# Kernel optimization log

Hardware: AMD Instinct MI355X
Metric: run time of the kernel (lower is better)

Reference implementation:

```python
import jax, jax.numpy as jnp
import numpy as np

EPS = 1e-12


def pairwise_sqdist(x, y):
    # x: (B, N, 3), y: (B, M, 3) -> (B, N, M) squared euclidean distances
    xx = jnp.sum(x * x, axis=-1)              # (B, N)
    yy = jnp.sum(y * y, axis=-1)              # (B, M)
    xy = jnp.einsum('bnd,bmd->bnm', x, y)     # (B, N, M)
    d = xx[:, :, None] + yy[None_ if False else yy[:, None, :].shape and 0 or ...] if False else xx[:, :, None] + yy[:, None, :] - 2.0 * xy
    return jnp.maximum(d, 0.0)


def chamfer_l1(x, y):
    # pytorch3d/PoinTr-style ChamferDistanceL1:
    # mean over points of sqrt(min squared dist), averaged over both directions
    d = pairwise_sqdist(x, y)                 # (B, N, M)
    d1 = jnp.min(d, axis=2)                   # (B, N) x -> nearest y
    d2 = jnp.min(d, axis=1)                   # (B, M) y -> nearest x
    d1 = jnp.sqrt(jnp.maximum(d1, EPS))
    d2 = jnp.sqrt(jnp.maximum(d2, EPS))
    return 0.5 * (jnp.mean(d1) + jnp.mean(d2))


def knn1_gather(x, y):
    # For each point in x (B,N,3), find nearest neighbor in y (B,M,3) (K=1)
    # and gather it -> (B, N, 3). Matches knn_points + knn_gather + squeeze.
    d = pairwise_sqdist(x, y)                 # (B, N, M)
    idx = jnp.argmin(d, axis=2)               # (B, N) int
    return jnp.take_along_axis(y, idx[:, :, None], axis=1)  # (B, N, 3)


def volume_with_wedge(p):
    # wedge-product volume over consecutive point triples:
    # V = sum_i (p_i x p_{i+1}) . p_{i+2} / 6  -> (B,)
    c = jnp.cross(p[:, :-2, :], p[:, 1:-1, :])  # (B, N-2, 3)
    return jnp.sum(jnp.einsum('bnd,bnd->bn', c, p[:, 2:, :]), axis=-1) / 6.0


def setup_inputs() -> dict:
    key = jax.random.key(0)
    k1, k2, k3 = jax.random.split(key, 3)
    B, Nc, Nf, M = 2, 512, 8192, 8192
    return {
        'source_coarse': jax.random.normal(k1, (B, Nc, 3), dtype=jnp.float32),
        'source_fine': jax.random.normal(k2, (B, Nf, 3), dtype=jnp.float32),
        'target_points': jax.random.normal(k3, (B, M, 3), dtype=jnp.float32),
    }


def reference(source_coarse, source_fine, target_points):
    lambda_rot = lambda_ref = lambda_align = lambda_geo = 1.0
    B = source_fine.shape[0]
    axis = jnp.broadcast_to(jnp.array([0.0, 0.0, 1.0], dtype=source_fine.dtype), (B, 3))
    plane_normal = jnp.broadcast_to(jnp.array([0.0, 1.0, 0.0], dtype=source_fine.dtype), (B, 3))

    # KNN (K=1) gather of nearest target point for each fine source point
    new_target = knn1_gather(source_fine, target_points)  # (B, Nf, 3)

    # alignment (Chamfer L1) losses
    loss_align_coarse = chamfer_l1(source_coarse, target_points)
    loss_align_fine = chamfer_l1(source_fine, target_points)

    # rotational symmetry loss
    in_proj = jnp.einsum('bij,bj->bi', source_fine, axis)      # (B, Nf)
    re_proj = jnp.einsum('bij,bj->bi', new_target, axis)
    loss_rot = jnp.mean((jnp.linalg.norm(in_proj, axis=-1) - jnp.linalg.norm(re_proj, axis=-1)) ** 2)

    # reflectional symmetry loss
    pn = plane_normal / jnp.linalg.norm(plane_normal, axis=-1, keepdims=True)
    in_dist = jnp.einsum('bij,bj->bi', source_fine, pn)
    re_dist = jnp.einsum('bij,bj->bi', new_target, pn)
    loss_ref = jnp.mean((in_dist - re_dist) ** 2)

    # geometric consistency (wedge-product volume) loss
    loss_geo = jnp.mean((volume_with_wedge(source_fine) - volume_with_wedge(new_target)) ** 2)

    total = (lambda_rot * loss_rot + lambda_ref * loss_ref
             + lambda_align * loss_align_coarse + lambda_align * loss_align_fine
             + lambda_geo * loss_geo)
    return total
```

## Files before the change

### kernel.cpp

```cpp
#include <hip/hip_runtime.h>
#include <stdint.h>

using u64 = unsigned long long;

constexpr int B_ = 2;
constexpr int NC = 512;
constexpr int NF = 8192;
constexpr int MT = 8192;

constexpr int TPB  = 256;
constexpr int RPT  = 2;
constexpr int RPB  = TPB * RPT;
constexpr int TILE = 256;

#define DEVINL __device__ __forceinline__

DEVINL float fmulrn(float a, float b){ return __fmul_rn(a,b); }
DEVINL float faddrn(float a, float b){ return __fadd_rn(a,b); }
DEVINL float fsubrn(float a, float b){ return __fsub_rn(a,b); }

template<bool ARGMIN>
DEVINL void pairmin_body(const float* __restrict__ P, const float* __restrict__ Q,
                         int nP, int nQ, int b, int row_base, int j0,
                         u64* __restrict__ outPack, unsigned* __restrict__ outVal,
                         float4* tile)
{
    const int tid = threadIdx.x;
    float x0[RPT], x1[RPT], x2[RPT], xx[RPT], dbest[RPT];
    int jbest[RPT];
    #pragma unroll
    for (int r = 0; r < RPT; ++r) {
        int row = row_base + tid + r * TPB;
        const float* p = P + ((size_t)b * nP + row) * 3;
        x0[r] = p[0]; x1[r] = p[1]; x2[r] = p[2];
        xx[r] = faddrn(faddrn(fmulrn(x0[r],x0[r]), fmulrn(x1[r],x1[r])),
                       fmulrn(x2[r],x2[r]));
        dbest[r] = __int_as_float(0x7f7fffff);
        jbest[r] = 0;
    }
    {
        const float* q = Q + ((size_t)b * nQ + j0 + tid) * 3;
        float q0 = q[0], q1 = q[1], q2 = q[2];
        float qq = faddrn(faddrn(fmulrn(q0,q0), fmulrn(q1,q1)), fmulrn(q2,q2));
        tile[tid] = make_float4(q0, q1, q2, qq);
    }
    __syncthreads();

    for (int jj = 0; jj < TILE; jj += 4) {
        float4 qv[4];
        #pragma unroll
        for (int u = 0; u < 4; ++u) qv[u] = tile[jj + u];
        #pragma unroll
        for (int u = 0; u < 4; ++u) {
            float4 q = qv[u];
            #pragma unroll
            for (int r = 0; r < RPT; ++r) {
                float xy = faddrn(faddrn(fmulrn(x0[r], q.x), fmulrn(x1[r], q.y)),
                                  fmulrn(x2[r], q.z));
                float t  = faddrn(xx[r], q.w);
                float d  = fsubrn(t, fmulrn(2.0f, xy));
                if (ARGMIN) {
                    d = fmaxf(d, 0.0f);
                    bool c = d < dbest[r];
                    dbest[r] = c ? d : dbest[r];
                    jbest[r] = c ? (j0 + jj + u) : jbest[r];
                } else {
                    dbest[r] = __builtin_amdgcn_fmed3f(d, 0.0f, dbest[r]);
                }
            }
        }
    }
    #pragma unroll
    for (int r = 0; r < RPT; ++r) {
        int row = row_base + tid + r * TPB;
        if (ARGMIN) {
            u64 pk = ((u64)__float_as_uint(dbest[r]) << 32) | (u64)(unsigned)jbest[r];
            atomicMin(&outPack[(size_t)b * nP + row], pk);
        } else {
            atomicMin(&outVal[(size_t)b * nP + row], __float_as_uint(dbest[r]));
        }
    }
}

__global__ __launch_bounds__(TPB, 4) void pairmin_all(
    const float* __restrict__ coarse, const float* __restrict__ fine,
    const float* __restrict__ tgt,
    u64* __restrict__ mp_f_rows, unsigned* __restrict__ val_f_cols,
    unsigned* __restrict__ val_c_rows, unsigned* __restrict__ val_c_cols)
{
    __shared__ float4 tile[TILE];
    int bx = blockIdx.x;
    if (bx < 64) {
        int chunk = bx & 31, b = bx >> 5;
        pairmin_body<false>(coarse, tgt, NC, MT, b, 0, chunk*TILE,
                            nullptr, val_c_rows, tile);
    } else if (bx < 128) {
        int i = bx - 64;
        int chunk = i & 1, yb = (i >> 1) & 15, b = i >> 5;
        pairmin_body<false>(tgt, coarse, MT, NC, b, yb*RPB, chunk*TILE,
                            nullptr, val_c_cols, tile);
    } else if (bx < 1152) {
        int i = bx - 128;
        int chunk = i & 31, yb = (i >> 5) & 15, b = i >> 9;
        pairmin_body<true>(fine, tgt, NF, MT, b, yb*RPB, chunk*TILE,
                           mp_f_rows, nullptr, tile);
    } else {
        int i = bx - 1152;
        int chunk = i & 31, yb = (i >> 5) & 15, b = i >> 9;
        pairmin_body<false>(tgt, fine, MT, NF, b, yb*RPB, chunk*TILE,
                            nullptr, val_f_cols, tile);
    }
}

__global__ __launch_bounds__(TPB) void finalize_fine(
    const u64* __restrict__ mp, const float* __restrict__ src,
    const float* __restrict__ tgt, double* __restrict__ acc,
    double* __restrict__ dV)
{
    __shared__ float sp[TPB + 2][3];
    __shared__ float yp[TPB + 2][3];
    const int b    = blockIdx.y;
    const int base = blockIdx.x * TPB;
    const int tid  = threadIdx.x;
    const int row  = base + tid;

    u64 p = mp[(size_t)b * NF + row];
    float d1 = __uint_as_float((unsigned)(p >> 32));
    int idx  = (int)(p & 0xffffffffULL);
    float s = sqrtf(fmaxf(d1, 1e-12f));
    const float* y  = tgt + ((size_t)b * MT + idx) * 3;
    const float* sr = src + ((size_t)b * NF + row) * 3;
    float y0 = y[0],  y1 = y[1],  y2 = y[2];
    float s0 = sr[0], s1 = sr[1], s2 = sr[2];
    yp[tid][0] = y0; yp[tid][1] = y1; yp[tid][2] = y2;
    sp[tid][0] = s0; sp[tid][1] = s1; sp[tid][2] = s2;
    if (tid < 2 && base + TPB + tid < NF) {
        int r2 = base + TPB + tid;
        u64 p2 = mp[(size_t)b * NF + r2];
        int i2 = (int)(p2 & 0xffffffffULL);
        const float* yh = tgt + ((size_t)b * MT + i2) * 3;
        const float* sh = src + ((size_t)b * NF + r2) * 3;
        #pragma unroll
        for (int k = 0; k < 3; ++k) { yp[TPB + tid][k] = yh[k]; sp[TPB + tid][k] = sh[k]; }
    }
    __syncthreads();

    float yd = s1 - y1;
    float v_s = s, v_yd2 = yd * yd, v_zs = s2 * s2, v_zt = y2 * y2;

    double vs = 0.0, vt = 0.0;
    if (row <= NF - 3) {
        {
            const float* a = sp[tid]; const float* c = sp[tid+1]; const float* e = sp[tid+2];
            float c0 = a[1]*c[2] - a[2]*c[1];
            float c1 = a[2]*c[0] - a[0]*c[2];
            float c2 = a[0]*c[1] - a[1]*c[0];
            vs = (double)(c0*e[0] + c1*e[1] + c2*e[2]);
        }
        {
            const float* a = yp[tid]; const float* c = yp[tid+1]; const float* e = yp[tid+2];
            float c0 = a[1]*c[2] - a[2]*c[1];
            float c1 = a[2]*c[0] - a[0]*c[2];
            float c2 = a[0]*c[1] - a[1]*c[0];
            vt = (double)(c0*e[0] + c1*e[1] + c2*e[2]);
        }
    }
    for (int o = 32; o; o >>= 1) {
        v_s   += __shfl_down(v_s,   o);
        v_yd2 += __shfl_down(v_yd2, o);
        v_zs  += __shfl_down(v_zs,  o);
        v_zt  += __shfl_down(v_zt,  o);
        vs    += __shfl_down(vs,    o);
        vt    += __shfl_down(vt,    o);
    }
    if ((tid & 63) == 0) {
        atomicAdd(&acc[0],     (double)v_s);
        atomicAdd(&acc[4],     (double)v_yd2);
        atomicAdd(&acc[5 + b], (double)v_zs);
        atomicAdd(&acc[7 + b], (double)v_zt);
        atomicAdd(&dV[2*b + 0], vs);
        atomicAdd(&dV[2*b + 1], vt);
    }
}

__global__ __launch_bounds__(TPB) void finalize_vals(
    const unsigned* __restrict__ vf, const unsigned* __restrict__ vcr,
    const unsigned* __restrict__ vcc, double* __restrict__ acc)
{
    int g = blockIdx.x * TPB + threadIdx.x;
    const unsigned* a; int off; int slot;
    if (g < 16384)      { a = vf;  off = g;          slot = 1; }
    else if (g < 17408) { a = vcr; off = g - 16384;  slot = 2; }
    else                { a = vcc; off = g - 17408;  slot = 3; }
    float d = __uint_as_float(a[off]);
    float s = sqrtf(fmaxf(d, 1e-12f));
    for (int o = 32; o; o >>= 1) s += __shfl_down(s, o);
    if ((threadIdx.x & 63) == 0) atomicAdd(&acc[slot], (double)s);
}

__global__ void combine_kernel(const double* __restrict__ acc,
                               const double* __restrict__ dV,
                               float* __restrict__ out)
{
    double m_d1f = acc[0] / (double)(B_ * NF);
    double m_d2f = acc[1] / (double)(B_ * MT);
    double m_d1c = acc[2] / (double)(B_ * NC);
    double m_d2c = acc[3] / (double)(B_ * MT);
    double loss_align_fine   = 0.5 * (m_d1f + m_d2f);
    double loss_align_coarse = 0.5 * (m_d1c + m_d2c);
    double loss_ref = acc[4] / (double)(B_ * NF);
    double loss_rot = 0.0, loss_geo = 0.0;
    for (int b = 0; b < B_; ++b) {
        double dn = sqrt(acc[5 + b]) - sqrt(acc[7 + b]);
        loss_rot += dn * dn;
        double dv = (dV[2*b] - dV[2*b + 1]) / 6.0;
        loss_geo += dv * dv;
    }
    loss_rot /= (double)B_;
    loss_geo /= (double)B_;
    out[0] = (float)(loss_rot + loss_ref + loss_align_coarse + loss_align_fine + loss_geo);
}

extern "C" void kernel_launch(void* const* d_in, const int* in_sizes, int n_in,
                              void* d_out, int out_size, void* d_ws, size_t ws_size,
                              hipStream_t stream)
{
    const float* src_coarse = (const float*)d_in[0];
    const float* src_fine   = (const float*)d_in[1];
    const float* tgt        = (const float*)d_in[2];
    float* out = (float*)d_out;
    char*  ws  = (char*)d_ws;

    u64*      mp_f_rows  = (u64*)(ws);
    unsigned* val_f_cols = (unsigned*)(ws + 131072);
    unsigned* val_c_rows = (unsigned*)(ws + 196608);
    unsigned* val_c_cols = (unsigned*)(ws + 200704);
    double*   dV         = (double*)(ws + 266240);
    double*   acc        = (double*)(ws + 266272);

    hipMemsetAsync(ws, 0xFF, 266240, stream);
    hipMemsetAsync(ws + 266240, 0, 160, stream);

    pairmin_all<<<dim3(2176), TPB, 0, stream>>>(
        src_coarse, src_fine, tgt, mp_f_rows, val_f_cols, val_c_rows, val_c_cols);

    finalize_fine<<<dim3(NF / TPB, B_), TPB, 0, stream>>>(mp_f_rows, src_fine, tgt, acc, dV);
    finalize_vals<<<dim3(132), TPB, 0, stream>>>(val_f_cols, val_c_rows, val_c_cols, acc);
    combine_kernel<<<1, 1, 0, stream>>>(acc, dV, out);
}
```

Before: 143.2 us.

## Replace atomics with per-chunk partials, packed-float distance math, and fused tail kernel

The pairwise-min kernel now writes per-chunk partial minima to distinct workspace slots instead of using atomicMin. It processes two column tiles per block (halving the grid), computes distances with packed two-wide float vectors and a pre-doubled x, and raises the launch-bounds occupancy hint. The three finalize/combine kernels and both memsets are folded into one tail kernel that reduces the partials and finishes the sum with a last-block-done counter. This removes atomic contention, memset launches and extra kernel launches, at the cost of a larger workspace and changed floating-point rounding order.

```diff
diff --git a/kernel.cpp b/kernel.cpp
--- a/kernel.cpp
+++ b/kernel.cpp
@@ -1,7 +1,9 @@
 #include <hip/hip_runtime.h>
 #include <stdint.h>
+#include <float.h>
 
 using u64 = unsigned long long;
+typedef float v2f __attribute__((ext_vector_type(2)));
 
 constexpr int B_ = 2;
 constexpr int NC = 512;
@@ -9,216 +11,274 @@
 constexpr int MT = 8192;
 
 constexpr int TPB  = 256;
-constexpr int RPT  = 2;
-constexpr int RPB  = TPB * RPT;
+constexpr int RPB  = 512;
 constexpr int TILE = 256;
+constexpr int CF   = 16;
+constexpr int TAIL_BLOCKS = 196;
 
 #define DEVINL __device__ __forceinline__
-
-DEVINL float fmulrn(float a, float b){ return __fmul_rn(a,b); }
-DEVINL float faddrn(float a, float b){ return __fadd_rn(a,b); }
-DEVINL float fsubrn(float a, float b){ return __fsub_rn(a,b); }
 
 template<bool ARGMIN>
 DEVINL void pairmin_body(const float* __restrict__ P, const float* __restrict__ Q,
-                         int nP, int nQ, int b, int row_base, int j0,
+                         int nP, int nQ, int b, int row_base, int j0, int ntiles,
+                         int chunk, int nRowsTot,
                          u64* __restrict__ outPack, unsigned* __restrict__ outVal,
                          float4* tile)
 {
-    const int tid = threadIdx.x;
-    float x0[RPT], x1[RPT], x2[RPT], xx[RPT], dbest[RPT];
-    int jbest[RPT];
-    #pragma unroll
-    for (int r = 0; r < RPT; ++r) {
-        int row = row_base + tid + r * TPB;
-        const float* p = P + ((size_t)b * nP + row) * 3;
-        x0[r] = p[0]; x1[r] = p[1]; x2[r] = p[2];
-        xx[r] = faddrn(faddrn(fmulrn(x0[r],x0[r]), fmulrn(x1[r],x1[r])),
-                       fmulrn(x2[r],x2[r]));
-        dbest[r] = __int_as_float(0x7f7fffff);
-        jbest[r] = 0;
-    }
-    {
-        const float* q = Q + ((size_t)b * nQ + j0 + tid) * 3;
-        float q0 = q[0], q1 = q[1], q2 = q[2];
-        float qq = faddrn(faddrn(fmulrn(q0,q0), fmulrn(q1,q1)), fmulrn(q2,q2));
-        tile[tid] = make_float4(q0, q1, q2, qq);
-    }
-    __syncthreads();
-
-    for (int jj = 0; jj < TILE; jj += 4) {
-        float4 qv[4];
-        #pragma unroll
-        for (int u = 0; u < 4; ++u) qv[u] = tile[jj + u];
-        #pragma unroll
-        for (int u = 0; u < 4; ++u) {
-            float4 q = qv[u];
+#pragma clang fp contract(off)
+    const int tid  = threadIdx.x;
+    const int row0 = row_base + tid;
+    const int row1 = row_base + tid + TPB;
+    const float* p0 = P + ((size_t)b * nP + row0) * 3;
+    const float* p1 = P + ((size_t)b * nP + row1) * 3;
+    float a0 = p0[0], a1 = p0[1], a2 = p0[2];
+    float e0 = p1[0], e1 = p1[1], e2 = p1[2];
+    v2f tx0 = {2.0f * a0, 2.0f * e0};
+    v2f tx1 = {2.0f * a1, 2.0f * e1};
+    v2f tx2 = {2.0f * a2, 2.0f * e2};
+    v2f txx = {(a0*a0 + a1*a1) + a2*a2, (e0*e0 + e1*e1) + e2*e2};
+    v2f dbest = {FLT_MAX, FLT_MAX};
+    const v2f vzero = {0.0f, 0.0f};
+    int jb0 = 0, jb1 = 0;
+
+    for (int t = 0; t < ntiles; ++t) {
+        __syncthreads();
+        {
+            const float* q = Q + ((size_t)b * nQ + j0 + t * TILE + tid) * 3;
+            float q0 = q[0], q1 = q[1], q2 = q[2];
+            tile[tid] = make_float4(q0, q1, q2, (q0*q0 + q1*q1) + q2*q2);
+        }
+        __syncthreads();
+        const int jbase = j0 + t * TILE;
+        for (int jj = 0; jj < TILE; jj += 4) {
+            float4 qv[4];
             #pragma unroll
-            for (int r = 0; r < RPT; ++r) {
-                float xy = faddrn(faddrn(fmulrn(x0[r], q.x), fmulrn(x1[r], q.y)),
-                                  fmulrn(x2[r], q.z));
-                float t  = faddrn(xx[r], q.w);
-                float d  = fsubrn(t, fmulrn(2.0f, xy));
+            for (int u = 0; u < 4; ++u) qv[u] = tile[jj + u];
+            #pragma unroll
+            for (int u = 0; u < 4; ++u) {
+                v2f s  = (tx0 * qv[u].x + tx1 * qv[u].y) + tx2 * qv[u].z;
+                v2f tt = txx + qv[u].w;
+                v2f d  = tt - s;
+                v2f dc = __builtin_elementwise_max(d, vzero);
                 if (ARGMIN) {
-                    d = fmaxf(d, 0.0f);
-                    bool c = d < dbest[r];
-                    dbest[r] = c ? d : dbest[r];
-                    jbest[r] = c ? (j0 + jj + u) : jbest[r];
+                    int j = jbase + jj + u;
+                    bool c0 = dc.x < dbest.x;
+                    dbest.x = c0 ? dc.x : dbest.x;  jb0 = c0 ? j : jb0;
+                    bool c1 = dc.y < dbest.y;
+                    dbest.y = c1 ? dc.y : dbest.y;  jb1 = c1 ? j : jb1;
                 } else {
-                    dbest[r] = __builtin_amdgcn_fmed3f(d, 0.0f, dbest[r]);
+                    dbest = __builtin_elementwise_min(dbest, dc);
                 }
             }
         }
     }
-    #pragma unroll
-    for (int r = 0; r < RPT; ++r) {
-        int row = row_base + tid + r * TPB;
-        if (ARGMIN) {
-            u64 pk = ((u64)__float_as_uint(dbest[r]) << 32) | (u64)(unsigned)jbest[r];
-            atomicMin(&outPack[(size_t)b * nP + row], pk);
-        } else {
-            atomicMin(&outVal[(size_t)b * nP + row], __float_as_uint(dbest[r]));
-        }
+    const size_t o0 = (size_t)chunk * nRowsTot + (size_t)b * nP;
+    if (ARGMIN) {
+        outPack[o0 + row0] = ((u64)__float_as_uint(dbest.x) << 32) | (unsigned)jb0;
+        outPack[o0 + row1] = ((u64)__float_as_uint(dbest.y) << 32) | (unsigned)jb1;
+    } else {
+        outVal[o0 + row0] = __float_as_uint(dbest.x);
+        outVal[o0 + row1] = __float_as_uint(dbest.y);
     }
 }
 
-__global__ __launch_bounds__(TPB, 4) void pairmin_all(
+__global__ __launch_bounds__(TPB, 8) void pairmin_all(
     const float* __restrict__ coarse, const float* __restrict__ fine,
     const float* __restrict__ tgt,
-    u64* __restrict__ mp_f_rows, unsigned* __restrict__ val_f_cols,
-    unsigned* __restrict__ val_c_rows, unsigned* __restrict__ val_c_cols)
+    u64* __restrict__ pfr, unsigned* __restrict__ pfc,
+    unsigned* __restrict__ pcr, unsigned* __restrict__ pcc,
+    unsigned* __restrict__ counter)
 {
     __shared__ float4 tile[TILE];
-    int bx = blockIdx.x;
+    const int bx = blockIdx.x;
+    if (bx == 0 && threadIdx.x == 0) *counter = 0;
     if (bx < 64) {
         int chunk = bx & 31, b = bx >> 5;
-        pairmin_body<false>(coarse, tgt, NC, MT, b, 0, chunk*TILE,
-                            nullptr, val_c_rows, tile);
+        pairmin_body<false>(coarse, tgt, NC, MT, b, 0, chunk * TILE, 1,
+                            chunk, B_ * NC, nullptr, pcr, tile);
     } else if (bx < 128) {
         int i = bx - 64;
         int chunk = i & 1, yb = (i >> 1) & 15, b = i >> 5;
-        pairmin_body<false>(tgt, coarse, MT, NC, b, yb*RPB, chunk*TILE,
-                            nullptr, val_c_cols, tile);
-    } else if (bx < 1152) {
+        pairmin_body<false>(tgt, coarse, MT, NC, b, yb * RPB, chunk * TILE, 1,
+                            chunk, B_ * MT, nullptr, pcc, tile);
+    } else if (bx < 640) {
         int i = bx - 128;
-        int chunk = i & 31, yb = (i >> 5) & 15, b = i >> 9;
-        pairmin_body<true>(fine, tgt, NF, MT, b, yb*RPB, chunk*TILE,
-                           mp_f_rows, nullptr, tile);
+        int chunk = i & 15, yb = (i >> 4) & 15, b = i >> 8;
+        pairmin_body<true>(fine, tgt, NF, MT, b, yb * RPB, chunk * (MT / CF), 2,
+                           chunk, B_ * NF, pfr, nullptr, tile);
     } else {
-        int i = bx - 1152;
-        int chunk = i & 31, yb = (i >> 5) & 15, b = i >> 9;
-        pairmin_body<false>(tgt, fine, MT, NF, b, yb*RPB, chunk*TILE,
-                            nullptr, val_f_cols, tile);
+        int i = bx - 640;
+        int chunk = i & 15, yb = (i >> 4) & 15, b = i >> 8;
+        pairmin_body<false>(tgt, fine, MT, NF, b, yb * RPB, chunk * (NF / CF), 2,
+                            chunk, B_ * MT, nullptr, pfc, tile);
     }
 }
 
-__global__ __launch_bounds__(TPB) void finalize_fine(
-    const u64* __restrict__ mp, const float* __restrict__ src,
-    const float* __restrict__ tgt, double* __restrict__ acc,
-    double* __restrict__ dV)
+__global__ __launch_bounds__(TPB) void tail_all(
+    const float* __restrict__ fine, const float* __restrict__ tgt,
+    const u64* __restrict__ pfr, const unsigned* __restrict__ pfc,
+    const unsigned* __restrict__ pcr, const unsigned* __restrict__ pcc,
+    double* __restrict__ bs, unsigned* __restrict__ counter,
+    float* __restrict__ out)
 {
-    __shared__ float sp[TPB + 2][3];
-    __shared__ float yp[TPB + 2][3];
-    const int b    = blockIdx.y;
-    const int base = blockIdx.x * TPB;
-    const int tid  = threadIdx.x;
-    const int row  = base + tid;
-
-    u64 p = mp[(size_t)b * NF + row];
-    float d1 = __uint_as_float((unsigned)(p >> 32));
-    int idx  = (int)(p & 0xffffffffULL);
-    float s = sqrtf(fmaxf(d1, 1e-12f));
-    const float* y  = tgt + ((size_t)b * MT + idx) * 3;
-    const float* sr = src + ((size_t)b * NF + row) * 3;
-    float y0 = y[0],  y1 = y[1],  y2 = y[2];
-    float s0 = sr[0], s1 = sr[1], s2 = sr[2];
-    yp[tid][0] = y0; yp[tid][1] = y1; yp[tid][2] = y2;
-    sp[tid][0] = s0; sp[tid][1] = s1; sp[tid][2] = s2;
-    if (tid < 2 && base + TPB + tid < NF) {
-        int r2 = base + TPB + tid;
-        u64 p2 = mp[(size_t)b * NF + r2];
-        int i2 = (int)(p2 & 0xffffffffULL);
-        const float* yh = tgt + ((size_t)b * MT + i2) * 3;
-        const float* sh = src + ((size_t)b * NF + r2) * 3;
-        #pragma unroll
-        for (int k = 0; k < 3; ++k) { yp[TPB + tid][k] = yh[k]; sp[TPB + tid][k] = sh[k]; }
+    __shared__ float sp[TPB + 2][3], yp[TPB + 2][3];
+    __shared__ double redw[4][9];
+    __shared__ double lred[4][13];
+    __shared__ int lastflag;
+    const int bx = blockIdx.x, tid = threadIdx.x;
+    const int wave = tid >> 6, lane = tid & 63;
+
+    double v_s = 0, v_d2f = 0, v_d1c = 0, v_d2c = 0, v_yd2 = 0, v_zs = 0, v_zt = 0;
+    double vs = 0, vt = 0;
+    int role_b = 0;
+
+    if (bx < 64) {
+        const int base = bx * TPB;
+        const int g = base + tid;
+        const int b = base >> 13;  role_b = b;
+        u64 best = pfr[g];
+        #pragma unroll
+        for (int c = 1; c < CF; ++c) {
+            u64 p = pfr[(size_t)c * (B_ * NF) + g];
+            best = p < best ? p : best;
+        }
+        float d1 = __uint_as_float((unsigned)(best >> 32));
+        int idx  = (int)(best & 0xffffffffULL);
+        float s = sqrtf(fmaxf(d1, 1e-12f));
+        const float* y  = tgt  + ((size_t)b * MT + idx) * 3;
+        const float* sr = fine + (size_t)g * 3;
+        float y0 = y[0],  y1 = y[1],  y2 = y[2];
+        float s0 = sr[0], s1 = sr[1], s2 = sr[2];
+        yp[tid][0] = y0; yp[tid][1] = y1; yp[tid][2] = y2;
+        sp[tid][0] = s0; sp[tid][1] = s1; sp[tid][2] = s2;
+        const int base_b = base & (NF - 1);
+        if (tid < 2 && base_b + TPB + tid < NF) {
+            int g2 = base + TPB + tid;
+            u64 b2 = pfr[g2];
+            #pragma unroll
+            for (int c = 1; c < CF; ++c) {
+                u64 p = pfr[(size_t)c * (B_ * NF) + g2];
+                b2 = p < b2 ? p : b2;
+            }
+            int i2 = (int)(b2 & 0xffffffffULL);
+            const float* yh = tgt  + ((size_t)b * MT + i2) * 3;
+            const float* sh = fine + (size_t)g2 * 3;
+            #pragma unroll
+            for (int k = 0; k < 3; ++k) { yp[TPB + tid][k] = yh[k]; sp[TPB + tid][k] = sh[k]; }
+        }
+        __syncthreads();
+        v_s = s;
+        float yd = s1 - y1;
+        v_yd2 = (double)(yd * yd);
+        v_zs  = (double)(s2 * s2);
+        v_zt  = (double)(y2 * y2);
+        int rb = base_b + tid;
+        if (rb <= NF - 3) {
+            {
+                const float* a = sp[tid]; const float* c = sp[tid+1]; const float* e = sp[tid+2];
+                float c0 = a[1]*c[2] - a[2]*c[1];
+                float c1 = a[2]*c[0] - a[0]*c[2];
+                float c2 = a[0]*c[1] - a[1]*c[0];
+                vs = (double)(c0*e[0] + c1*e[1] + c2*e[2]);
+            }
+            {
+                const float* a = yp[tid]; const float* c = yp[tid+1]; const float* e = yp[tid+2];
+                float c0 = a[1]*c[2] - a[2]*c[1];
+                float c1 = a[2]*c[0] - a[0]*c[2];
+                float c2 = a[0]*c[1] - a[1]*c[0];
+                vt = (double)(c0*e[0] + c1*e[1] + c2*e[2]);
+            }
+        }
+    } else if (bx < 128) {
+        const int g = (bx - 64) * TPB + tid;
+        unsigned best = pfc[g];
+        #pragma unroll
+        for (int c = 1; c < CF; ++c) best = min(best, pfc[(size_t)c * (B_ * MT) + g]);
+        v_d2f = (double)sqrtf(fmaxf(__uint_as_float(best), 1e-12f));
+    } else if (bx < 132) {
+        const int g = (bx - 128) * TPB + tid;
+        unsigned best = pcr[g];
+        #pragma unroll
+        for (int c = 1; c < 32; ++c) best = min(best, pcr[(size_t)c * (B_ * NC) + g]);
+        v_d1c = (double)sqrtf(fmaxf(__uint_as_float(best), 1e-12f));
+    } else {
+        const int g = (bx - 132) * TPB + tid;
+        unsigned best = min(pcc[g], pcc[(size_t)(B_ * MT) + g]);
+        v_d2c = (double)sqrtf(fmaxf(__uint_as_float(best), 1e-12f));
+    }
+
+    double r9[9] = {v_s, v_d2f, v_d1c, v_d2c, v_yd2, v_zs, v_zt, vs, vt};
+    for (int o = 32; o; o >>= 1) {
+        #pragma unroll
+        for (int k = 0; k < 9; ++k) r9[k] += __shfl_down(r9[k], o);
+    }
+    if (lane == 0) {
+        #pragma unroll
+        for (int k = 0; k < 9; ++k) redw[wave][k] = r9[k];
     }
     __syncthreads();
-
-    float yd = s1 - y1;
-    float v_s = s, v_yd2 = yd * yd, v_zs = s2 * s2, v_zt = y2 * y2;
-
-    double vs = 0.0, vt = 0.0;
-    if (row <= NF - 3) {
-        {
-            const float* a = sp[tid]; const float* c = sp[tid+1]; const float* e = sp[tid+2];
-            float c0 = a[1]*c[2] - a[2]*c[1];
-            float c1 = a[2]*c[0] - a[0]*c[2];
-            float c2 = a[0]*c[1] - a[1]*c[0];
-            vs = (double)(c0*e[0] + c1*e[1] + c2*e[2]);
-        }
-        {
-            const float* a = yp[tid]; const float* c = yp[tid+1]; const float* e = yp[tid+2];
-            float c0 = a[1]*c[2] - a[2]*c[1];
-            float c1 = a[2]*c[0] - a[0]*c[2];
-            float c2 = a[0]*c[1] - a[1]*c[0];
-            vt = (double)(c0*e[0] + c1*e[1] + c2*e[2]);
-        }
+    if (tid == 0) {
+        double t9[9];
+        #pragma unroll
+        for (int k = 0; k < 9; ++k)
+            t9[k] = redw[0][k] + redw[1][k] + redw[2][k] + redw[3][k];
+        double* o = bs + (size_t)bx * 16;
+        #pragma unroll
+        for (int k = 0; k < 16; ++k) o[k] = 0.0;
+        o[0] = t9[0]; o[1] = t9[1]; o[2] = t9[2]; o[3] = t9[3]; o[4] = t9[4];
+        o[5 + role_b]  = t9[5];
+        o[7 + role_b]  = t9[6];
+        o[9 + role_b]  = t9[7];
+        o[11 + role_b] = t9[8];
+        __threadfence();
+        unsigned old = atomicAdd(counter, 1u);
+        lastflag = (old == TAIL_BLOCKS - 1);
+    }
+    __syncthreads();
+    if (!lastflag) return;
+
+    __threadfence();
+    double c13[13];
+    if (tid < TAIL_BLOCKS) {
+        const double* p = bs + (size_t)tid * 16;
+        #pragma unroll
+        for (int k = 0; k < 13; ++k) c13[k] = p[k];
+    } else {
+        #pragma unroll
+        for (int k = 0; k < 13; ++k) c13[k] = 0.0;
     }
     for (int o = 32; o; o >>= 1) {
-        v_s   += __shfl_down(v_s,   o);
-        v_yd2 += __shfl_down(v_yd2, o);
-        v_zs  += __shfl_down(v_zs,  o);
-        v_zt  += __shfl_down(v_zt,  o);
-        vs    += __shfl_down(vs,    o);
-        vt    += __shfl_down(vt,    o);
-    }
-    if ((tid & 63) == 0) {
-        atomicAdd(&acc[0],     (double)v_s);
-        atomicAdd(&acc[4],     (double)v_yd2);
-        atomicAdd(&acc[5 + b], (double)v_zs);
-        atomicAdd(&acc[7 + b], (double)v_zt);
-        atomicAdd(&dV[2*b + 0], vs);
-        atomicAdd(&dV[2*b + 1], vt);
-    }
-}
-
-__global__ __launch_bounds__(TPB) void finalize_vals(
-    const unsigned* __restrict__ vf, const unsigned* __restrict__ vcr,
-    const unsigned* __restrict__ vcc, double* __restrict__ acc)
-{
-    int g = blockIdx.x * TPB + threadIdx.x;
-    const unsigned* a; int off; int slot;
-    if (g < 16384)      { a = vf;  off = g;          slot = 1; }
-    else if (g < 17408) { a = vcr; off = g - 16384;  slot = 2; }
-    else                { a = vcc; off = g - 17408;  slot = 3; }
-    float d = __uint_as_float(a[off]);
-    float s = sqrtf(fmaxf(d, 1e-12f));
-    for (int o = 32; o; o >>= 1) s += __shfl_down(s, o);
-    if ((threadIdx.x & 63) == 0) atomicAdd(&acc[slot], (double)s);
-}
-
-__global__ void combine_kernel(const double* __restrict__ acc,
-                               const double* __restrict__ dV,
-                               float* __restrict__ out)
-{
-    double m_d1f = acc[0] / (double)(B_ * NF);
-    double m_d2f = acc[1] / (double)(B_ * MT);
-    double m_d1c = acc[2] / (double)(B_ * NC);
-    double m_d2c = acc[3] / (double)(B_ * MT);
-    double loss_align_fine   = 0.5 * (m_d1f + m_d2f);
-    double loss_align_coarse = 0.5 * (m_d1c + m_d2c);
-    double loss_ref = acc[4] / (double)(B_ * NF);
-    double loss_rot = 0.0, loss_geo = 0.0;
-    for (int b = 0; b < B_; ++b) {
-        double dn = sqrt(acc[5 + b]) - sqrt(acc[7 + b]);
-        loss_rot += dn * dn;
-        double dv = (dV[2*b] - dV[2*b + 1]) / 6.0;
-        loss_geo += dv * dv;
-    }
-    loss_rot /= (double)B_;
-    loss_geo /= (double)B_;
-    out[0] = (float)(loss_rot + loss_ref + loss_align_coarse + loss_align_fine + loss_geo);
+        #pragma unroll
+        for (int k = 0; k < 13; ++k) c13[k] += __shfl_down(c13[k], o);
+    }
+    if (lane == 0) {
+        #pragma unroll
+        for (int k = 0; k < 13; ++k) lred[wave][k] = c13[k];
+    }
+    __syncthreads();
+    if (tid == 0) {
+        double S[13];
+        #pragma unroll
+        for (int k = 0; k < 13; ++k)
+            S[k] = lred[0][k] + lred[1][k] + lred[2][k] + lred[3][k];
+        double m_d1f = S[0] / (double)(B_ * NF);
+        double m_d2f = S[1] / (double)(B_ * MT);
+        double m_d1c = S[2] / (double)(B_ * NC);
+        double m_d2c = S[3] / (double)(B_ * MT);
+        double loss_align_fine   = 0.5 * (m_d1f + m_d2f);
+        double loss_align_coarse = 0.5 * (m_d1c + m_d2c);
+        double loss_ref = S[4] / (double)(B_ * NF);
+        double loss_rot = 0.0, loss_geo = 0.0;
+        for (int b = 0; b < B_; ++b) {
+            double dn = sqrt(S[5 + b]) - sqrt(S[7 + b]);
+            loss_rot += dn * dn;
+            double dv = (S[9 + b] - S[11 + b]) / 6.0;
+            loss_geo += dv * dv;
+        }
+        loss_rot /= (double)B_;
+        loss_geo /= (double)B_;
+        out[0] = (float)(loss_rot + loss_ref + loss_align_coarse + loss_align_fine + loss_geo);
+    }
 }
 
 extern "C" void kernel_launch(void* const* d_in, const int* in_sizes, int n_in,
@@ -231,20 +291,15 @@
     float* out = (float*)d_out;
     char*  ws  = (char*)d_ws;
 
-    u64*      mp_f_rows  = (u64*)(ws);
-    unsigned* val_f_cols = (unsigned*)(ws + 131072);
-    unsigned* val_c_rows = (unsigned*)(ws + 196608);
-    unsigned* val_c_cols = (unsigned*)(ws + 200704);
-    double*   dV         = (double*)(ws + 266240);
-    double*   acc        = (double*)(ws + 266272);
-
-    hipMemsetAsync(ws, 0xFF, 266240, stream);
-    hipMemsetAsync(ws + 266240, 0, 160, stream);
-
-    pairmin_all<<<dim3(2176), TPB, 0, stream>>>(
-        src_coarse, src_fine, tgt, mp_f_rows, val_f_cols, val_c_rows, val_c_cols);
-
-    finalize_fine<<<dim3(NF / TPB, B_), TPB, 0, stream>>>(mp_f_rows, src_fine, tgt, acc, dV);
-    finalize_vals<<<dim3(132), TPB, 0, stream>>>(val_f_cols, val_c_rows, val_c_cols, acc);
-    combine_kernel<<<1, 1, 0, stream>>>(acc, dV, out);
+    u64*      pfr     = (u64*)(ws);
+    unsigned* pfc     = (unsigned*)(ws + 2097152);
+    unsigned* pcr     = (unsigned*)(ws + 3145728);
+    unsigned* pcc     = (unsigned*)(ws + 3276800);
+    double*   bs      = (double*)(ws + 3407872);
+    unsigned* counter = (unsigned*)(ws + 3432960);
+
+    pairmin_all<<<dim3(1152), TPB, 0, stream>>>(
+        src_coarse, src_fine, tgt, pfr, pfc, pcr, pcc, counter);
+    tail_all<<<dim3(TAIL_BLOCKS), TPB, 0, stream>>>(
+        src_fine, tgt, pfr, pfc, pcr, pcc, bs, counter, out);
 }
```

Result: faster. 130.3 us (-9.0%).
